# Kernel tuning notes

Hardware: AMD Instinct MI355X
Metric: run time of the kernel (lower is better)

The kernel has to match this reference:

```python
import jax, jax.numpy as jnp
import numpy as np

B, T_OBS, T_FUT, D, H = 8192, 128, 64, 5, 128


def _gru_step(h, x, Wih, Whh, bih, bhh):
    # PyTorch GRU math, gate order (r, z, n) in the stacked [3H, *] weights.
    gi = x @ Wih.T + bih          # [B, 3H]
    gh = h @ Whh.T + bhh          # [B, 3H]
    ir, iz, inn = jnp.split(gi, 3, axis=-1)
    hr, hz, hn = jnp.split(gh, 3, axis=-1)
    r = jax.nn.sigmoid(ir + hr)
    z = jax.nn.sigmoid(iz + hz)
    n = jnp.tanh(inn + r * hn)
    return (1.0 - z) * n + z * h


def setup_inputs() -> dict:
    key = jax.random.key(0)
    ks = jax.random.split(key, 12)
    s = 0.1  # modest init scale to keep gates in a sane range
    return {
        "obs": jax.random.normal(ks[0], (B, T_OBS, D), jnp.float32),
        "target": jax.random.normal(ks[1], (B, T_FUT, D), jnp.float32),
        "enc_Wih": jax.random.normal(ks[2], (3 * H, D), jnp.float32) * s,
        "enc_Whh": jax.random.normal(ks[3], (3 * H, H), jnp.float32) * s,
        "enc_bih": jax.random.normal(ks[4], (3 * H,), jnp.float32) * s,
        "enc_bhh": jax.random.normal(ks[5], (3 * H,), jnp.float32) * s,
        "cell_Wih": jax.random.normal(ks[6], (3 * H, D), jnp.float32) * s,
        "cell_Whh": jax.random.normal(ks[7], (3 * H, H), jnp.float32) * s,
        "cell_bih": jax.random.normal(ks[8], (3 * H,), jnp.float32) * s,
        "cell_bhh": jax.random.normal(ks[9], (3 * H,), jnp.float32) * s,
        "head_W": jax.random.normal(ks[10], (D, H), jnp.float32) * s,
        "head_b": jax.random.normal(ks[11], (D,), jnp.float32) * s,
    }


def reference(obs, target, enc_Wih, enc_Whh, enc_bih, enc_bhh,
              cell_Wih, cell_Whh, cell_bih, cell_bhh, head_W, head_b):
    b = obs.shape[0]
    h0 = jnp.zeros((b, H), obs.dtype)

    # --- encoder: GRU over obs, keep only final hidden state ---
    def enc_step(h, x):
        h_new = _gru_step(h, x, enc_Wih, enc_Whh, enc_bih, enc_bhh)
        return h_new, None
    hT, _ = jax.lax.scan(enc_step, h0, jnp.swapaxes(obs, 0, 1))  # xs: [T_obs, B, D]

    # --- teacher-forced rollout: x_0 = obs[:, -1], x_t = target[:, t-1] ---
    xs = jnp.concatenate([obs[:, -1:, :], target[:, :-1, :]], axis=1)  # [B, T_fut, D]
    def roll_step(h, x):
        h_new = _gru_step(h, x, cell_Wih, cell_Whh, cell_bih, cell_bhh)
        return h_new, h_new
    _, hs = jax.lax.scan(roll_step, hT, jnp.swapaxes(xs, 0, 1))  # hs: [T_fut, B, H]

    preds = jnp.einsum('tbh,dh->tbd', hs, head_W) + head_b  # [T_fut, B, D]
    return jnp.swapaxes(preds, 0, 1)  # [B, T_fut, D]
```

## Files before the change

kernel.cpp:

```cpp
#include <hip/hip_runtime.h>

#define B_TOT 8192
#define T_OBS 128
#define T_FUT 64
#define T_ALL 192
#define DIN 5
#define HD 128
#define BT 32
#define LDSTR 136

typedef __attribute__((ext_vector_type(8))) short short8;
typedef __attribute__((ext_vector_type(4))) float f32x4;

__device__ inline short f2bf(float f) {
    unsigned u = __float_as_uint(f);
    u += 0x7FFFu + ((u >> 16) & 1u);
    return (short)(u >> 16);
}

__device__ inline float sigm(float x) {
    return __builtin_amdgcn_rcpf(1.f + __expf(-x));
}
__device__ inline float tanh_(float x) {
    return 1.f - 2.f * __builtin_amdgcn_rcpf(1.f + __expf(2.f * x));
}

__device__ inline f32x4 MFMA(short8 a, short8 b, f32x4 c) {
    return __builtin_amdgcn_mfma_f32_16x16x32_bf16(a, b, c, 0, 0, 0);
}

__device__ inline short8 load_w8(const float* p) {
    float4 a = *reinterpret_cast<const float4*>(p);
    float4 b = *reinterpret_cast<const float4*>(p + 4);
    short8 r;
    r[0] = f2bf(a.x); r[1] = f2bf(a.y); r[2] = f2bf(a.z); r[3] = f2bf(a.w);
    r[4] = f2bf(b.x); r[5] = f2bf(b.y); r[6] = f2bf(b.z); r[7] = f2bf(b.w);
    return r;
}
__device__ inline short8 load_w5(const float* p) {
    short8 r = (short8)0;
    r[0] = f2bf(p[0]); r[1] = f2bf(p[1]); r[2] = f2bf(p[2]);
    r[3] = f2bf(p[3]); r[4] = f2bf(p[4]);
    return r;
}

__global__ __launch_bounds__(512, 2)
void gru_tracemodel_kernel(const float* __restrict__ obs, const float* __restrict__ target,
                           const float* __restrict__ eWih, const float* __restrict__ eWhh,
                           const float* __restrict__ ebih, const float* __restrict__ ebhh,
                           const float* __restrict__ cWih, const float* __restrict__ cWhh,
                           const float* __restrict__ cbih, const float* __restrict__ cbhh,
                           const float* __restrict__ headW, const float* __restrict__ headb,
                           float* __restrict__ out)
{
    __shared__ __attribute__((aligned(16))) short Abuf[2][BT][LDSTR];

    const int tid   = threadIdx.x;
    const int wave  = tid >> 6;
    const int lane  = tid & 63;
    const int q     = lane >> 4;
    const int c     = lane & 15;
    const int b0    = blockIdx.x * BT;
    const int wbase = wave * 16;

    for (int i = tid; i < 2 * BT * LDSTR; i += 512) ((short*)Abuf)[i] = 0;

    short8 Wr[5], Wz[5], Wn[5];
    float  br, bz, bnh_, bni_;

    auto load_phase = [&](const float* Wih, const float* Whh,
                          const float* bih, const float* bhh) {
        const int nr = 0 * HD + wbase + c;
        const int nz = 1 * HD + wbase + c;
        const int nn = 2 * HD + wbase + c;
        #pragma unroll
        for (int kt = 0; kt < 4; ++kt) {
            Wr[kt] = load_w8(Whh + nr * HD + kt * 32 + q * 8);
            Wz[kt] = load_w8(Whh + nz * HD + kt * 32 + q * 8);
            Wn[kt] = load_w8(Whh + nn * HD + kt * 32 + q * 8);
        }
        Wr[4] = (q == 0) ? load_w5(Wih + nr * DIN) : (short8)0;
        Wz[4] = (q == 0) ? load_w5(Wih + nz * DIN) : (short8)0;
        Wn[4] = (q == 0) ? load_w5(Wih + nn * DIN) : (short8)0;
        br   = bih[nr] + bhh[nr];
        bz   = bih[nz] + bhh[nz];
        bnh_ = bhh[nn];
        bni_ = bih[nn];
    };
    load_phase(eWih, eWhh, ebih, ebhh);

    short8 Whd[4];
    float  hb = 0.f;
    if (wave == 0) {
        #pragma unroll
        for (int kt = 0; kt < 4; ++kt)
            Whd[kt] = (c < DIN) ? load_w8(headW + c * HD + kt * 32 + q * 8) : (short8)0;
        hb = (c < DIN) ? headb[c] : 0.f;
    }

    float hreg[2][4] = {{0.f,0.f,0.f,0.f},{0.f,0.f,0.f,0.f}};

    const float* obsr[2] = { obs + (size_t)(b0 + c) * (T_OBS * DIN),
                             obs + (size_t)(b0 + 16 + c) * (T_OBS * DIN) };
    const float* tgtr[2] = { target + (size_t)(b0 + c) * (T_FUT * DIN),
                             target + (size_t)(b0 + 16 + c) * (T_FUT * DIN) };
    float x5[2][5] = {{0,0,0,0,0},{0,0,0,0,0}};
    if (q == 0) {
        #pragma unroll
        for (int a = 0; a < 2; ++a)
            #pragma unroll
            for (int j = 0; j < DIN; ++j) x5[a][j] = obsr[a][j];
    }

    for (int t = 0; t <= T_ALL; ++t) {
        __syncthreads();
        const int p = t & 1;

        short8 ah[2][4];
        #pragma unroll
        for (int a = 0; a < 2; ++a) {
            const short* ap = &Abuf[p][a * 16 + c][0];
            #pragma unroll
            for (int kt = 0; kt < 4; ++kt)
                ah[a][kt] = *reinterpret_cast<const short8*>(ap + kt * 32 + q * 8);
        }

        if (wave == 0 && t >= T_OBS + 1) {
            const int s = t - (T_OBS + 1);
            #pragma unroll
            for (int a = 0; a < 2; ++a) {
                f32x4 acc = {hb, hb, hb, hb};
                #pragma unroll
                for (int kt = 0; kt < 4; ++kt)
                    acc = MFMA(ah[a][kt], Whd[kt], acc);
                if (c < DIN) {
                    #pragma unroll
                    for (int r = 0; r < 4; ++r) {
                        int m = a * 16 + q * 4 + r;
                        out[((size_t)(b0 + m) * T_FUT + s) * DIN + c] = acc[r];
                    }
                }
            }
        }
        if (t == T_ALL) break;

        if (t == T_OBS) load_phase(cWih, cWhh, cbih, cbhh);

        short8 ax[2] = {(short8)0, (short8)0};
        if (q == 0) {
            #pragma unroll
            for (int a = 0; a < 2; ++a)
                #pragma unroll
                for (int j = 0; j < DIN; ++j) ax[a][j] = f2bf(x5[a][j]);
            const int tn = t + 1;
            if (tn < T_ALL) {
                #pragma unroll
                for (int a = 0; a < 2; ++a) {
                    const float* px = (tn < T_OBS)  ? (obsr[a] + tn * DIN)
                                    : (tn == T_OBS) ? (obsr[a] + (T_OBS - 1) * DIN)
                                                    : (tgtr[a] + (tn - T_OBS - 1) * DIN);
                    #pragma unroll
                    for (int j = 0; j < DIN; ++j) x5[a][j] = px[j];
                }
            }
        }

        f32x4 aR[2], aZ[2], aNh[2], aNi[2];
        #pragma unroll
        for (int a = 0; a < 2; ++a) {
            aR[a]  = {br, br, br, br};
            aZ[a]  = {bz, bz, bz, bz};
            aNh[a] = {bnh_, bnh_, bnh_, bnh_};
            aNi[a] = {bni_, bni_, bni_, bni_};
            #pragma unroll
            for (int kt = 0; kt < 4; ++kt) {
                aR[a]  = MFMA(ah[a][kt], Wr[kt], aR[a]);
                aZ[a]  = MFMA(ah[a][kt], Wz[kt], aZ[a]);
                aNh[a] = MFMA(ah[a][kt], Wn[kt], aNh[a]);
            }
            aR[a]  = MFMA(ax[a], Wr[4], aR[a]);
            aZ[a]  = MFMA(ax[a], Wz[4], aZ[a]);
            aNi[a] = MFMA(ax[a], Wn[4], aNi[a]);
        }

        #pragma unroll
        for (int a = 0; a < 2; ++a)
            #pragma unroll
            for (int r = 0; r < 4; ++r) {
                float rv = sigm(aR[a][r]);
                float zv = sigm(aZ[a][r]);
                float nv = tanh_(aNi[a][r] + rv * aNh[a][r]);
                float hn = nv + zv * (hreg[a][r] - nv);
                hreg[a][r] = hn;
                Abuf[1 - p][a * 16 + q * 4 + r][wbase + c] = f2bf(hn);
            }
    }
}

extern "C" void kernel_launch(void* const* d_in, const int* in_sizes, int n_in,
                              void* d_out, int out_size, void* d_ws, size_t ws_size,
                              hipStream_t stream)
{
    (void)in_sizes; (void)n_in; (void)d_ws; (void)ws_size; (void)out_size;
    gru_tracemodel_kernel<<<dim3(B_TOT / BT), dim3(512), 0, stream>>>(
        (const float*)d_in[0],  (const float*)d_in[1],
        (const float*)d_in[2],  (const float*)d_in[3],
        (const float*)d_in[4],  (const float*)d_in[5],
        (const float*)d_in[6],  (const float*)d_in[7],
        (const float*)d_in[8],  (const float*)d_in[9],
        (const float*)d_in[10], (const float*)d_in[11],
        (float*)d_out);
}
```

Measured before the change: 401.8 us.

## Transpose MFMA operands for packed LDS stores, fold log2e into weights, rotate head wave

The gate MFMAs swap operand order so each lane holds four consecutive hidden units of one batch row. The new hidden state is packed with v_cvt_pk_bf16_f32 and written to LDS as one 8-byte store instead of four scalar short stores. Weights and biases are pre-scaled by log2(e) (and 2*log2(e) for the n gate), so activations use raw exp2 without an extra multiply. The output-head projection now rotates across waves each step instead of always landing on wave 0, and launch bounds are relaxed to one block per SM, which may raise register use. Folding the scale into bf16 weights changes rounding slightly.

```diff
diff --git a/kernel.cpp b/kernel.cpp
--- a/kernel.cpp
+++ b/kernel.cpp
@@ -9,8 +9,12 @@
 #define BT 32
 #define LDSTR 136
 
+#define LOG2E 1.44269504088896340736f
+
 typedef __attribute__((ext_vector_type(8))) short short8;
 typedef __attribute__((ext_vector_type(4))) float f32x4;
+typedef __attribute__((ext_vector_type(2))) unsigned int u32x2;
+typedef __attribute__((ext_vector_type(4))) unsigned int u32x4;
 
 __device__ inline short f2bf(float f) {
     unsigned u = __float_as_uint(f);
@@ -18,33 +22,32 @@
     return (short)(u >> 16);
 }
 
-__device__ inline float sigm(float x) {
-    return __builtin_amdgcn_rcpf(1.f + __expf(-x));
-}
-__device__ inline float tanh_(float x) {
-    return 1.f - 2.f * __builtin_amdgcn_rcpf(1.f + __expf(2.f * x));
+__device__ inline unsigned cvtpk(float lo, float hi) {
+    unsigned r;
+    asm volatile("v_cvt_pk_bf16_f32 %0, %1, %2" : "=v"(r) : "v"(lo), "v"(hi));
+    return r;
 }
 
 __device__ inline f32x4 MFMA(short8 a, short8 b, f32x4 c) {
     return __builtin_amdgcn_mfma_f32_16x16x32_bf16(a, b, c, 0, 0, 0);
 }
 
-__device__ inline short8 load_w8(const float* p) {
+__device__ inline short8 load_w8s(const float* p, float s) {
     float4 a = *reinterpret_cast<const float4*>(p);
     float4 b = *reinterpret_cast<const float4*>(p + 4);
     short8 r;
-    r[0] = f2bf(a.x); r[1] = f2bf(a.y); r[2] = f2bf(a.z); r[3] = f2bf(a.w);
-    r[4] = f2bf(b.x); r[5] = f2bf(b.y); r[6] = f2bf(b.z); r[7] = f2bf(b.w);
+    r[0] = f2bf(a.x * s); r[1] = f2bf(a.y * s); r[2] = f2bf(a.z * s); r[3] = f2bf(a.w * s);
+    r[4] = f2bf(b.x * s); r[5] = f2bf(b.y * s); r[6] = f2bf(b.z * s); r[7] = f2bf(b.w * s);
     return r;
 }
-__device__ inline short8 load_w5(const float* p) {
+__device__ inline short8 load_w5s(const float* p, float s) {
     short8 r = (short8)0;
-    r[0] = f2bf(p[0]); r[1] = f2bf(p[1]); r[2] = f2bf(p[2]);
-    r[3] = f2bf(p[3]); r[4] = f2bf(p[4]);
+    r[0] = f2bf(p[0] * s); r[1] = f2bf(p[1] * s); r[2] = f2bf(p[2] * s);
+    r[3] = f2bf(p[3] * s); r[4] = f2bf(p[4] * s);
     return r;
 }
 
-__global__ __launch_bounds__(512, 2)
+__global__ __launch_bounds__(512, 1)
 void gru_tracemodel_kernel(const float* __restrict__ obs, const float* __restrict__ target,
                            const float* __restrict__ eWih, const float* __restrict__ eWhh,
                            const float* __restrict__ ebih, const float* __restrict__ ebhh,
@@ -66,7 +69,7 @@
     for (int i = tid; i < 2 * BT * LDSTR; i += 512) ((short*)Abuf)[i] = 0;
 
     short8 Wr[5], Wz[5], Wn[5];
-    float  br, bz, bnh_, bni_;
+    f32x4  br4, bz4, bnh4, bni4;
 
     auto load_phase = [&](const float* Wih, const float* Whh,
                           const float* bih, const float* bhh) {
@@ -75,28 +78,32 @@
         const int nn = 2 * HD + wbase + c;
         #pragma unroll
         for (int kt = 0; kt < 4; ++kt) {
-            Wr[kt] = load_w8(Whh + nr * HD + kt * 32 + q * 8);
-            Wz[kt] = load_w8(Whh + nz * HD + kt * 32 + q * 8);
-            Wn[kt] = load_w8(Whh + nn * HD + kt * 32 + q * 8);
-        }
-        Wr[4] = (q == 0) ? load_w5(Wih + nr * DIN) : (short8)0;
-        Wz[4] = (q == 0) ? load_w5(Wih + nz * DIN) : (short8)0;
-        Wn[4] = (q == 0) ? load_w5(Wih + nn * DIN) : (short8)0;
-        br   = bih[nr] + bhh[nr];
-        bz   = bih[nz] + bhh[nz];
-        bnh_ = bhh[nn];
-        bni_ = bih[nn];
+            Wr[kt] = load_w8s(Whh + nr * HD + kt * 32 + q * 8, LOG2E);
+            Wz[kt] = load_w8s(Whh + nz * HD + kt * 32 + q * 8, LOG2E);
+            Wn[kt] = load_w8s(Whh + nn * HD + kt * 32 + q * 8, 2.f * LOG2E);
+        }
+        Wr[4] = (q == 0) ? load_w5s(Wih + nr * DIN, LOG2E) : (short8)0;
+        Wz[4] = (q == 0) ? load_w5s(Wih + nz * DIN, LOG2E) : (short8)0;
+        Wn[4] = (q == 0) ? load_w5s(Wih + nn * DIN, 2.f * LOG2E) : (short8)0;
+        const int n0 = wbase + q * 4;
+        #pragma unroll
+        for (int r = 0; r < 4; ++r) {
+            br4[r]  = (bih[0 * HD + n0 + r] + bhh[0 * HD + n0 + r]) * LOG2E;
+            bz4[r]  = (bih[1 * HD + n0 + r] + bhh[1 * HD + n0 + r]) * LOG2E;
+            bni4[r] = bih[2 * HD + n0 + r] * (2.f * LOG2E);
+            bnh4[r] = bhh[2 * HD + n0 + r] * (2.f * LOG2E);
+        }
     };
     load_phase(eWih, eWhh, ebih, ebhh);
 
     short8 Whd[4];
-    float  hb = 0.f;
-    if (wave == 0) {
-        #pragma unroll
-        for (int kt = 0; kt < 4; ++kt)
-            Whd[kt] = (c < DIN) ? load_w8(headW + c * HD + kt * 32 + q * 8) : (short8)0;
-        hb = (c < DIN) ? headb[c] : 0.f;
-    }
+    f32x4  hb4;
+    #pragma unroll
+    for (int kt = 0; kt < 4; ++kt)
+        Whd[kt] = (c < DIN) ? load_w8s(headW + c * HD + kt * 32 + q * 8, 1.f) : (short8)0;
+    #pragma unroll
+    for (int r = 0; r < 4; ++r)
+        hb4[r] = (q * 4 + r < DIN) ? headb[q * 4 + r] : 0.f;
 
     float hreg[2][4] = {{0.f,0.f,0.f,0.f},{0.f,0.f,0.f,0.f}};
 
@@ -125,20 +132,19 @@
                 ah[a][kt] = *reinterpret_cast<const short8*>(ap + kt * 32 + q * 8);
         }
 
-        if (wave == 0 && t >= T_OBS + 1) {
+        if (t >= T_OBS + 1 && wave == ((t - T_OBS - 1) & 7)) {
             const int s = t - (T_OBS + 1);
+            const int d0 = q * 4;
             #pragma unroll
             for (int a = 0; a < 2; ++a) {
-                f32x4 acc = {hb, hb, hb, hb};
+                f32x4 acc = hb4;
                 #pragma unroll
                 for (int kt = 0; kt < 4; ++kt)
-                    acc = MFMA(ah[a][kt], Whd[kt], acc);
-                if (c < DIN) {
-                    #pragma unroll
-                    for (int r = 0; r < 4; ++r) {
-                        int m = a * 16 + q * 4 + r;
-                        out[((size_t)(b0 + m) * T_FUT + s) * DIN + c] = acc[r];
-                    }
+                    acc = MFMA(Whd[kt], ah[a][kt], acc);
+                if (d0 < DIN) {
+                    float* op = out + ((size_t)(b0 + a * 16 + c) * T_FUT + s) * DIN + d0;
+                    op[0] = acc[0];
+                    if (q == 0) { op[1] = acc[1]; op[2] = acc[2]; op[3] = acc[3]; }
                 }
             }
         }
@@ -146,14 +152,23 @@
 
         if (t == T_OBS) load_phase(cWih, cWhh, cbih, cbhh);
 
-        short8 ax[2] = {(short8)0, (short8)0};
-        if (q == 0) {
-            #pragma unroll
-            for (int a = 0; a < 2; ++a)
-                #pragma unroll
-                for (int j = 0; j < DIN; ++j) ax[a][j] = f2bf(x5[a][j]);
+        short8 ax[2];
+        {
+            unsigned u0a = 0, u1a = 0, u2a = 0, u0b = 0, u1b = 0, u2b = 0;
+            if (q == 0) {
+                u0a = cvtpk(x5[0][0], x5[0][1]);
+                u1a = cvtpk(x5[0][2], x5[0][3]);
+                u2a = cvtpk(x5[0][4], 0.f);
+                u0b = cvtpk(x5[1][0], x5[1][1]);
+                u1b = cvtpk(x5[1][2], x5[1][3]);
+                u2b = cvtpk(x5[1][4], 0.f);
+            }
+            u32x4 va = {u0a, u1a, u2a, 0u};
+            u32x4 vb = {u0b, u1b, u2b, 0u};
+            ax[0] = __builtin_bit_cast(short8, va);
+            ax[1] = __builtin_bit_cast(short8, vb);
             const int tn = t + 1;
-            if (tn < T_ALL) {
+            if (q == 0 && tn < T_ALL) {
                 #pragma unroll
                 for (int a = 0; a < 2; ++a) {
                     const float* px = (tn < T_OBS)  ? (obsr[a] + tn * DIN)
@@ -165,35 +180,36 @@
             }
         }
 
-        f32x4 aR[2], aZ[2], aNh[2], aNi[2];
         #pragma unroll
         for (int a = 0; a < 2; ++a) {
-            aR[a]  = {br, br, br, br};
-            aZ[a]  = {bz, bz, bz, bz};
-            aNh[a] = {bnh_, bnh_, bnh_, bnh_};
-            aNi[a] = {bni_, bni_, bni_, bni_};
+            f32x4 aR  = br4;
+            f32x4 aZ  = bz4;
+            f32x4 aNh = bnh4;
+            f32x4 aNi = bni4;
             #pragma unroll
             for (int kt = 0; kt < 4; ++kt) {
-                aR[a]  = MFMA(ah[a][kt], Wr[kt], aR[a]);
-                aZ[a]  = MFMA(ah[a][kt], Wz[kt], aZ[a]);
-                aNh[a] = MFMA(ah[a][kt], Wn[kt], aNh[a]);
-            }
-            aR[a]  = MFMA(ax[a], Wr[4], aR[a]);
-            aZ[a]  = MFMA(ax[a], Wz[4], aZ[a]);
-            aNi[a] = MFMA(ax[a], Wn[4], aNi[a]);
-        }
-
-        #pragma unroll
-        for (int a = 0; a < 2; ++a)
+                aR  = MFMA(Wr[kt], ah[a][kt], aR);
+                aZ  = MFMA(Wz[kt], ah[a][kt], aZ);
+                aNh = MFMA(Wn[kt], ah[a][kt], aNh);
+            }
+            aR  = MFMA(Wr[4], ax[a], aR);
+            aZ  = MFMA(Wz[4], ax[a], aZ);
+            aNi = MFMA(Wn[4], ax[a], aNi);
+
+            float hn[4];
             #pragma unroll
             for (int r = 0; r < 4; ++r) {
-                float rv = sigm(aR[a][r]);
-                float zv = sigm(aZ[a][r]);
-                float nv = tanh_(aNi[a][r] + rv * aNh[a][r]);
-                float hn = nv + zv * (hreg[a][r] - nv);
-                hreg[a][r] = hn;
-                Abuf[1 - p][a * 16 + q * 4 + r][wbase + c] = f2bf(hn);
-            }
+                float rv = __builtin_amdgcn_rcpf(1.f + __builtin_amdgcn_exp2f(-aR[r]));
+                float zv = __builtin_amdgcn_rcpf(1.f + __builtin_amdgcn_exp2f(-aZ[r]));
+                float yv = fmaf(rv, aNh[r], aNi[r]);
+                float nv = 1.f - 2.f * __builtin_amdgcn_rcpf(1.f + __builtin_amdgcn_exp2f(yv));
+                float h_ = nv + zv * (hreg[a][r] - nv);
+                hreg[a][r] = h_;
+                hn[r] = h_;
+            }
+            u32x2 wv = { cvtpk(hn[0], hn[1]), cvtpk(hn[2], hn[3]) };
+            *reinterpret_cast<u32x2*>(&Abuf[1 - p][a * 16 + c][wbase + q * 4]) = wv;
+        }
     }
 }
 
```

New measurement: 338.1 us. -15.8%, faster.
